# Kernel optimization log

Hardware: AMD Instinct MI355X
Metric: run time of the kernel (lower is better)

Reference implementation:

```python
import jax, jax.numpy as jnp
import numpy as np


def setup_inputs() -> dict:
    B, Lq, Lk, D, F, H = 2, 2048, 2048, 128, 128, 8
    key = jax.random.key(0)
    ks = jax.random.split(key, 8)
    X_Q = jax.random.normal(ks[0], (B, Lq, D), dtype=jnp.float32)
    X_K = jax.random.normal(ks[1], (B, Lk, D), dtype=jnp.float32)
    X_V = jax.random.normal(ks[2], (B, Lk, F), dtype=jnp.float32)
    mask = jax.random.randint(ks[3], (B, 1, Lq, Lk), 0, 2, dtype=jnp.int32)
    # xavier_normal for [H, D, D]: std = sqrt(2/(D+D))
    W_Q = jax.random.normal(ks[4], (H, D, D), dtype=jnp.float32) * np.sqrt(2.0 / (D + D))
    W_K = jax.random.normal(ks[5], (H, D, D), dtype=jnp.float32) * np.sqrt(2.0 / (D + D))
    W_V = jax.random.normal(ks[6], (H, F, F), dtype=jnp.float32) * np.sqrt(2.0 / (F + F))
    O = jax.random.normal(ks[7], (F * H, F), dtype=jnp.float32) * np.sqrt(2.0 / (F * H + F))
    return {"X_Q": X_Q, "X_K": X_K, "X_V": X_V, "mask": mask,
            "W_Q": W_Q, "W_K": W_K, "W_V": W_V, "O": O}


def reference(X_Q, X_K, X_V, mask, W_Q, W_K, W_V, O):
    B, Lq, D = X_Q.shape
    H = W_Q.shape[0]
    F = W_V.shape[1]
    # torch.einsum with repeated in-operand index ('hdd') takes the diagonal
    dq = jnp.diagonal(W_Q, axis1=1, axis2=2)  # [H, D]
    dk = jnp.diagonal(W_K, axis1=1, axis2=2)  # [H, D]
    dv = jnp.diagonal(W_V, axis1=1, axis2=2)  # [H, F]
    g = dq * dk                               # fused per-head QK diagonal scale [H, D]
    scale = 1.0 / jnp.sqrt(jnp.asarray(D, dtype=X_Q.dtype))
    scores = jnp.einsum('bqd,hd,bkd->bhqk', X_Q, g, X_K) * scale  # [B,H,Lq,Lk]
    scores = jnp.where(mask == 0, jnp.asarray(-jnp.inf, scores.dtype), scores)
    A = jax.nn.softmax(scores, axis=-1)
    # O_h = A @ (diag(dv_h) scaled V)
    Oh = jnp.einsum('bhqk,hf,bkf->bhqf', A, dv, X_V)  # [B,H,Lq,F]
    Oh = Oh.transpose(0, 2, 1, 3).reshape(B, Lq, H * F)
    return jnp.einsum('bqx,xf->bqf', Oh, O)
```

## Files before the change

### kernel.cpp

```cpp
#include <hip/hip_runtime.h>

typedef __bf16 bf16;
typedef __bf16 bf16x4 __attribute__((ext_vector_type(4)));
typedef __bf16 bf16x8 __attribute__((ext_vector_type(8)));
typedef float f32x4 __attribute__((ext_vector_type(4)));
typedef short s16x4 __attribute__((ext_vector_type(4)));
typedef unsigned int u32;
typedef unsigned long long u64;

#define B_ 2
#define H_ 8
#define L_ 2048
#define D_ 128
#define F_ 128
#define QT 64
#define KT 64
#define NKT (L_ / KT)

#define WS_KB 0u
#define WS_VT (1u << 20)
#define WS_MB (2u << 20)

#define SMEM_BYTES 66048
#define LWS_OFF 65536
#define POX_STRIDE 132
#define SOH_OFF 36864
#define SOH_STRIDE 136
#define SO2_STRIDE 136

__device__ __forceinline__ void dma16(const void* g, void* l) {
    __builtin_amdgcn_global_load_lds(
        (const __attribute__((address_space(1))) u32*)g,
        (__attribute__((address_space(3))) u32*)l, 16, 0, 0);
}

__device__ __forceinline__ f32x4 mfma32(bf16x8 a, bf16x8 b, f32x4 c) {
    return __builtin_amdgcn_mfma_f32_16x16x32_bf16(a, b, c, 0, 0, 0);
}

__device__ __forceinline__ f32x4 mfma16(bf16x4 a, bf16x4 b, f32x4 c) {
#if __has_builtin(__builtin_amdgcn_mfma_f32_16x16x16_bf16)
    return __builtin_amdgcn_mfma_f32_16x16x16_bf16(a, b, c, 0, 0, 0);
#else
    s16x4 as = __builtin_bit_cast(s16x4, a);
    s16x4 bs = __builtin_bit_cast(s16x4, b);
    return __builtin_amdgcn_mfma_f32_16x16x16bf16_1k(as, bs, c, 0, 0, 0);
#endif
}

__global__ __launch_bounds__(256)
void prep_all(const float* __restrict__ XK, const float* __restrict__ XV,
              const int* __restrict__ mask, bf16* __restrict__ Kb,
              bf16* __restrict__ Vtb, u64* __restrict__ bits)
{
    const int bid = blockIdx.x;
    const int tid = threadIdx.x;
    if (bid < 8192) {
        int wv = bid * 4 + (tid >> 6);
        int lane = tid & 63;
        size_t base = (size_t)wv * 256;
        #pragma unroll
        for (int s = 0; s < 4; ++s) {
            int m = mask[base + s * 64 + lane];
            u64 bal = __ballot(m != 0);
            if (lane == 0) bits[(size_t)wv * 4 + s] = bal;
        }
    } else if (bid < 8448) {
        int gid = (bid - 8192) * 256 + tid;
        int row = gid >> 4;
        int j   = gid & 15;
        const float* src = XK + (size_t)row * 128 + j * 8;
        float4 v0 = *(const float4*)src;
        float4 v1 = *(const float4*)(src + 4);
        bf16x8 w;
        w[0] = (bf16)v0.x; w[1] = (bf16)v0.y; w[2] = (bf16)v0.z; w[3] = (bf16)v0.w;
        w[4] = (bf16)v1.x; w[5] = (bf16)v1.y; w[6] = (bf16)v1.z; w[7] = (bf16)v1.w;
        int jp = j ^ (row & 15);
        *(bf16x8*)(Kb + (size_t)row * 128 + jp * 8) = w;
    } else {
        int idx  = bid - 8448;
        int tile = idx >> 2;
        int fq   = idx & 3;
        int f    = fq * 32 + (tid & 31);
        int j    = tid >> 5;
        int bb   = tile >> 5, kt = tile & 31;
        const float* src = XV + ((size_t)(bb * L_ + kt * 64 + j * 8)) * F_ + f;
        bf16x4 w0, w1;
        #pragma unroll
        for (int jj = 0; jj < 4; ++jj) {
            w0[jj] = (bf16)src[(size_t)jj * F_];
            w1[jj] = (bf16)src[(size_t)(4 + jj) * F_];
        }
        bf16* outp = Vtb + (size_t)tile * 8192 + f * 64;
        *(bf16x4*)(outp + (((2 * j) ^ (f & 15)) * 4)) = w0;
        *(bf16x4*)(outp + (((2 * j + 1) ^ (f & 15)) * 4)) = w1;
    }
}

__global__ __launch_bounds__(512, 4)
void attn_fused_kernel(const float* __restrict__ XQ, const bf16* __restrict__ Kb,
                       const bf16* __restrict__ Vtb, const u64* __restrict__ bits,
                       const float* __restrict__ WQ, const float* __restrict__ WK,
                       const float* __restrict__ WV, const float* __restrict__ Om,
                       float* __restrict__ out)
{
    __shared__ __align__(16) char smem[SMEM_BYTES];
    __shared__ __align__(16) float g_s[128];

    bf16* sK0 = (bf16*)smem;
    bf16* sK1 = (bf16*)(smem + 16384);
    bf16* sV0 = (bf16*)(smem + 32768);
    bf16* sV1 = (bf16*)(smem + 49152);
    float* lws = (float*)(smem + LWS_OFF);
    float* pOx = (float*)smem;
    bf16* sOh  = (bf16*)(smem + SOH_OFF);
    bf16* sO2t = (bf16*)smem;

    const int tid  = threadIdx.x;
    const int wave = tid >> 6;
    const int lane = tid & 63;
    const int c    = lane & 15;
    const int quad = lane >> 4;
    const int qt = blockIdx.x, h = blockIdx.y, b = blockIdx.z;
    const int q0 = qt * QT;

    const int kh   = wave >> 2;
    const int msel = wave & 3;
    const int fv  = tid & 127;
    const int grp = tid >> 7;

    if (tid < 128) {
        float wq = WQ[(h * D_ + tid) * D_ + tid];
        float wk = WK[(h * D_ + tid) * D_ + tid];
        g_s[tid] = wq * wk * 0.08838834764831845f;
    }
    __syncthreads();

    const char* gKbase = (const char*)Kb + (size_t)(b * L_) * 256;
    const char* gVbase = (const char*)Vtb + (size_t)(b * NKT) * 16384;

    #pragma unroll
    for (int i = 0; i < 2; ++i) dma16(gKbase + i * 8192 + tid * 16, (char*)sK0 + i * 8192 + tid * 16);
    #pragma unroll
    for (int i = 0; i < 2; ++i) dma16(gVbase + i * 8192 + tid * 16, (char*)sV0 + i * 8192 + tid * 16);

    bf16x8 qfrag[4];
    {
        const float* qrow = XQ + (size_t)(b * L_ + q0 + msel * 16 + c) * D_;
        #pragma unroll
        for (int kc = 0; kc < 4; ++kc) {
            int d0 = kc * 32 + quad * 8;
            float4 v0 = *(const float4*)(qrow + d0);
            float4 v1 = *(const float4*)(qrow + d0 + 4);
            float4 g0 = *(const float4*)(g_s + d0);
            float4 g1 = *(const float4*)(g_s + d0 + 4);
            bf16x8 w;
            w[0] = (bf16)(v0.x * g0.x); w[1] = (bf16)(v0.y * g0.y);
            w[2] = (bf16)(v0.z * g0.z); w[3] = (bf16)(v0.w * g0.w);
            w[4] = (bf16)(v1.x * g1.x); w[5] = (bf16)(v1.y * g1.y);
            w[6] = (bf16)(v1.z * g1.z); w[7] = (bf16)(v1.w * g1.w);
            qfrag[kc] = w;
        }
    }

    f32x4 oacc[8];
    #pragma unroll
    for (int fi = 0; fi < 8; ++fi)
        #pragma unroll
        for (int r = 0; r < 4; ++r) oacc[fi][r] = 0.f;
    float lsum = 0.f;

    const u64* mrow = bits + (size_t)(b * L_ + q0 + msel * 16 + c) * NKT;

    #pragma unroll 2
    for (int kt = 0; kt < NKT; ++kt) {
        bf16* sK  = (kt & 1) ? sK1 : sK0;
        bf16* sV  = (kt & 1) ? sV1 : sV0;
        bf16* sKn = (kt & 1) ? sK0 : sK1;
        bf16* sVn = (kt & 1) ? sV0 : sV1;

        asm volatile("s_barrier" ::: "memory");

        u64 mb = mrow[kt];

        if (kt + 1 < NKT) {
            const char* gk = gKbase + (size_t)(kt + 1) * 16384;
            const char* gv = gVbase + (size_t)(kt + 1) * 16384;
            #pragma unroll
            for (int i = 0; i < 2; ++i) dma16(gk + i * 8192 + tid * 16, (char*)sKn + i * 8192 + tid * 16);
            #pragma unroll
            for (int i = 0; i < 2; ++i) dma16(gv + i * 8192 + tid * 16, (char*)sVn + i * 8192 + tid * 16);
            asm volatile("s_waitcnt vmcnt(5)" ::: "memory");
        } else {
            asm volatile("s_waitcnt vmcnt(1)" ::: "memory");
        }
        asm volatile("s_barrier" ::: "memory");

        f32x4 tacc[2];
        #pragma unroll
        for (int kti = 0; kti < 2; ++kti)
            #pragma unroll
            for (int r = 0; r < 4; ++r) tacc[kti][r] = 0.f;

        #pragma unroll
        for (int kti = 0; kti < 2; ++kti) {
            const bf16* krow = sK + ((kh * 2 + kti) * 16 + c) * 128;
            #pragma unroll
            for (int kc = 0; kc < 4; ++kc) {
                bf16x8 kfrag = *(const bf16x8*)(krow + (((kc * 4 + quad) ^ c) * 8));
                tacc[kti] = mfma32(kfrag, qfrag[kc], tacc[kti]);
            }
        }

        bf16x4 pfrag[2];
        #pragma unroll
        for (int kti = 0; kti < 2; ++kti) {
            #pragma unroll
            for (int r = 0; r < 4; ++r) {
                float p = ((mb >> (kh * 32 + kti * 16 + quad * 4 + r)) & 1ull)
                          ? __expf(tacc[kti][r]) : 0.f;
                lsum += p;
                pfrag[kti][r] = (bf16)p;
            }
        }

        #pragma unroll
        for (int fi = 0; fi < 8; ++fi) {
            #pragma unroll
            for (int kti = 0; kti < 2; ++kti) {
                int g = kh * 8 + kti * 4 + quad;
                bf16x4 vfrag = *(const bf16x4*)(sV + (fi * 16 + c) * 64 + ((g ^ c) * 4));
                oacc[fi] = mfma16(pfrag[kti], vfrag, oacc[fi]);
            }
        }
    }

    {
        float v = lsum;
        v += __shfl_xor(v, 16); v += __shfl_xor(v, 32);
        if (lane < 16) lws[wave * 16 + lane] = v;
    }
    if (tid < 128)
        g_s[tid] = WV[(h * F_ + tid) * F_ + tid];
    __syncthreads();

    if (kh == 1) {
        #pragma unroll
        for (int fi = 0; fi < 8; ++fi)
            #pragma unroll
            for (int r = 0; r < 4; ++r)
                pOx[(msel * 16 + quad * 4 + r) * POX_STRIDE + fi * 16 + c] = oacc[fi][r];
    }
    __syncthreads();

    if (kh == 0) {
        float linv[4];
        #pragma unroll
        for (int r = 0; r < 4; ++r) {
            int m16 = quad * 4 + r;
            linv[r] = 1.0f / (lws[msel * 16 + m16] + lws[(4 + msel) * 16 + m16]);
        }
        #pragma unroll
        for (int fi = 0; fi < 8; ++fi)
            #pragma unroll
            for (int r = 0; r < 4; ++r) {
                int row = msel * 16 + quad * 4 + r;
                float v = (oacc[fi][r] + pOx[row * POX_STRIDE + fi * 16 + c]) * linv[r];
                sOh[row * SOH_STRIDE + fi * 16 + c] = (bf16)v;
            }
    }
    __syncthreads();

    #pragma unroll
    for (int i = 0; i < 8; ++i) {
        int fp4 = grp * 32 + i * 4;
        bf16x4 w;
        #pragma unroll
        for (int j = 0; j < 4; ++j) {
            int x = fp4 + j;
            w[j] = (bf16)(Om[(h * F_ + x) * F_ + fv] * g_s[x]);
        }
        *(bf16x4*)(sO2t + fv * SO2_STRIDE + fp4) = w;
    }
    __syncthreads();

    const int pm = wave & 3;
    const int pf = wave >> 2;
    bf16x8 afr[4];
    const bf16* ohrow = sOh + (pm * 16 + c) * SOH_STRIDE;
    #pragma unroll
    for (int kc = 0; kc < 4; ++kc)
        afr[kc] = *(const bf16x8*)(ohrow + kc * 32 + quad * 8);

    #pragma unroll
    for (int nt = 0; nt < 4; ++nt) {
        f32x4 pacc;
        #pragma unroll
        for (int r = 0; r < 4; ++r) pacc[r] = 0.f;
        const bf16* orow = sO2t + ((pf * 4 + nt) * 16 + c) * SO2_STRIDE;
        #pragma unroll
        for (int kc = 0; kc < 4; ++kc) {
            bf16x8 bfrag = *(const bf16x8*)(orow + kc * 32 + quad * 8);
            pacc = mfma32(afr[kc], bfrag, pacc);
        }
        #pragma unroll
        for (int r = 0; r < 4; ++r) {
            int qg = q0 + pm * 16 + quad * 4 + r;
            atomicAdd(out + ((size_t)(b * L_ + qg) * F_ + (pf * 4 + nt) * 16 + c), pacc[r]);
        }
    }
}

extern "C" void kernel_launch(void* const* d_in, const int* in_sizes, int n_in,
                              void* d_out, int out_size, void* d_ws, size_t ws_size,
                              hipStream_t stream) {
    const float* XQ   = (const float*)d_in[0];
    const float* XK   = (const float*)d_in[1];
    const float* XV   = (const float*)d_in[2];
    const int*   mask = (const int*)d_in[3];
    const float* WQ   = (const float*)d_in[4];
    const float* WK   = (const float*)d_in[5];
    const float* WV   = (const float*)d_in[6];
    const float* Om   = (const float*)d_in[7];
    float* out = (float*)d_out;

    char* ws = (char*)d_ws;
    bf16* Kb   = (bf16*)(ws + WS_KB);
    bf16* Vtb  = (bf16*)(ws + WS_VT);
    u64*  bits = (u64*)(ws + WS_MB);

    prep_all<<<8704, 256, 0, stream>>>(XK, XV, mask, Kb, Vtb, bits);
    hipMemsetAsync(out, 0, (size_t)out_size * sizeof(float), stream);

    dim3 grid(L_ / QT, H_, B_);
    attn_fused_kernel<<<grid, 512, 0, stream>>>(XQ, Kb, Vtb, bits, WQ, WK, WV, Om, out);
}
```

Baseline: 156.0 us.

## Double query tile per block, load V fragments directly to registers, use exp2

Result: slower. 180.8 us (+15.9%).

```diff
diff --git a/kernel.cpp b/kernel.cpp
--- a/kernel.cpp
+++ b/kernel.cpp
@@ -13,20 +13,22 @@
 #define L_ 2048
 #define D_ 128
 #define F_ 128
-#define QT 64
+#define QT 128
 #define KT 64
 #define NKT (L_ / KT)
+#define NQT (L_ / QT)
 
 #define WS_KB 0u
 #define WS_VT (1u << 20)
 #define WS_MB (2u << 20)
 
-#define SMEM_BYTES 66048
-#define LWS_OFF 65536
+#define SMEM_BYTES 136192
+#define POX_OFF 32768
 #define POX_STRIDE 132
-#define SOH_OFF 36864
+#define SOH_OFF 100352
 #define SOH_STRIDE 136
 #define SO2_STRIDE 136
+#define LWS_OFF 135168
 
 __device__ __forceinline__ void dma16(const void* g, void* l) {
     __builtin_amdgcn_global_load_lds(
@@ -45,6 +47,14 @@
     s16x4 as = __builtin_bit_cast(s16x4, a);
     s16x4 bs = __builtin_bit_cast(s16x4, b);
     return __builtin_amdgcn_mfma_f32_16x16x16bf16_1k(as, bs, c, 0, 0, 0);
+#endif
+}
+
+__device__ __forceinline__ float fast_exp2(float x) {
+#if __has_builtin(__builtin_amdgcn_exp2f)
+    return __builtin_amdgcn_exp2f(x);
+#else
+    return exp2f(x);
 #endif
 }
 
@@ -78,26 +88,29 @@
         int jp = j ^ (row & 15);
         *(bf16x8*)(Kb + (size_t)row * 128 + jp * 8) = w;
     } else {
-        int idx  = bid - 8448;
-        int tile = idx >> 2;
-        int fq   = idx & 3;
-        int f    = fq * 32 + (tid & 31);
-        int j    = tid >> 5;
-        int bb   = tile >> 5, kt = tile & 31;
-        const float* src = XV + ((size_t)(bb * L_ + kt * 64 + j * 8)) * F_ + f;
-        bf16x4 w0, w1;
-        #pragma unroll
-        for (int jj = 0; jj < 4; ++jj) {
-            w0[jj] = (bf16)src[(size_t)jj * F_];
-            w1[jj] = (bf16)src[(size_t)(4 + jj) * F_];
-        }
-        bf16* outp = Vtb + (size_t)tile * 8192 + f * 64;
-        *(bf16x4*)(outp + (((2 * j) ^ (f & 15)) * 4)) = w0;
-        *(bf16x4*)(outp + (((2 * j + 1) ^ (f & 15)) * 4)) = w1;
-    }
-}
-
-__global__ __launch_bounds__(512, 4)
+        int tile = bid - 8448;
+        int bb = tile >> 5, kt = tile & 31;
+        #pragma unroll
+        for (int i = 0; i < 4; ++i) {
+            int idx  = tid * 4 + i;
+            int fblk = idx >> 6;
+            int lane = idx & 63;
+            int c = lane & 15, quad = lane >> 4;
+            int fi = fblk >> 1, kh = fblk & 1;
+            int f = fi * 16 + c;
+            int kb = kt * 64 + kh * 32 + quad * 4;
+            bf16x8 w;
+            #pragma unroll
+            for (int j = 0; j < 4; ++j) {
+                w[j]     = (bf16)XV[(size_t)(bb * L_ + kb + j) * F_ + f];
+                w[4 + j] = (bf16)XV[(size_t)(bb * L_ + kb + 16 + j) * F_ + f];
+            }
+            *(bf16x8*)(Vtb + (size_t)tile * 8192 + fblk * 512 + lane * 8) = w;
+        }
+    }
+}
+
+__global__ __launch_bounds__(512, 2)
 void attn_fused_kernel(const float* __restrict__ XQ, const bf16* __restrict__ Kb,
                        const bf16* __restrict__ Vtb, const u64* __restrict__ bits,
                        const float* __restrict__ WQ, const float* __restrict__ WK,
@@ -107,14 +120,12 @@
     __shared__ __align__(16) char smem[SMEM_BYTES];
     __shared__ __align__(16) float g_s[128];
 
-    bf16* sK0 = (bf16*)smem;
-    bf16* sK1 = (bf16*)(smem + 16384);
-    bf16* sV0 = (bf16*)(smem + 32768);
-    bf16* sV1 = (bf16*)(smem + 49152);
+    bf16* sK0  = (bf16*)smem;
+    bf16* sK1  = (bf16*)(smem + 16384);
+    float* pOx = (float*)(smem + POX_OFF);
+    bf16* sO2t = (bf16*)(smem + POX_OFF);
+    bf16* sOh  = (bf16*)(smem + SOH_OFF);
     float* lws = (float*)(smem + LWS_OFF);
-    float* pOx = (float*)smem;
-    bf16* sOh  = (bf16*)(smem + SOH_OFF);
-    bf16* sO2t = (bf16*)smem;
 
     const int tid  = threadIdx.x;
     const int wave = tid >> 6;
@@ -132,21 +143,20 @@
     if (tid < 128) {
         float wq = WQ[(h * D_ + tid) * D_ + tid];
         float wk = WK[(h * D_ + tid) * D_ + tid];
-        g_s[tid] = wq * wk * 0.08838834764831845f;
-    }
-    __syncthreads();
-
-    const char* gKbase = (const char*)Kb + (size_t)(b * L_) * 256;
-    const char* gVbase = (const char*)Vtb + (size_t)(b * NKT) * 16384;
-
-    #pragma unroll
-    for (int i = 0; i < 2; ++i) dma16(gKbase + i * 8192 + tid * 16, (char*)sK0 + i * 8192 + tid * 16);
-    #pragma unroll
-    for (int i = 0; i < 2; ++i) dma16(gVbase + i * 8192 + tid * 16, (char*)sV0 + i * 8192 + tid * 16);
-
-    bf16x8 qfrag[4];
-    {
-        const float* qrow = XQ + (size_t)(b * L_ + q0 + msel * 16 + c) * D_;
+        g_s[tid] = wq * wk * 0.12752230502179406f;
+    }
+    __syncthreads();
+
+    const char* gK = (const char*)Kb + (size_t)(b * L_) * 256;
+    const char* gV = (const char*)Vtb + (size_t)(b * NKT) * 16384;
+
+    dma16(gK + tid * 16, (char*)sK0 + tid * 16);
+    dma16(gK + 8192 + tid * 16, (char*)sK0 + 8192 + tid * 16);
+
+    bf16x8 qfrag[2][4];
+    #pragma unroll
+    for (int mi = 0; mi < 2; ++mi) {
+        const float* qrow = XQ + (size_t)(b * L_ + q0 + msel * 32 + mi * 16 + c) * D_;
         #pragma unroll
         for (int kc = 0; kc < 4; ++kc) {
             int d0 = kc * 32 + quad * 8;
@@ -159,48 +169,56 @@
             w[2] = (bf16)(v0.z * g0.z); w[3] = (bf16)(v0.w * g0.w);
             w[4] = (bf16)(v1.x * g1.x); w[5] = (bf16)(v1.y * g1.y);
             w[6] = (bf16)(v1.z * g1.z); w[7] = (bf16)(v1.w * g1.w);
-            qfrag[kc] = w;
-        }
-    }
-
-    f32x4 oacc[8];
-    #pragma unroll
-    for (int fi = 0; fi < 8; ++fi)
-        #pragma unroll
-        for (int r = 0; r < 4; ++r) oacc[fi][r] = 0.f;
-    float lsum = 0.f;
-
-    const u64* mrow = bits + (size_t)(b * L_ + q0 + msel * 16 + c) * NKT;
+            qfrag[mi][kc] = w;
+        }
+    }
+
+    f32x4 oacc[2][8];
+    #pragma unroll
+    for (int mi = 0; mi < 2; ++mi)
+        #pragma unroll
+        for (int fi = 0; fi < 8; ++fi)
+            #pragma unroll
+            for (int r = 0; r < 4; ++r) oacc[mi][fi][r] = 0.f;
+    float lsum[2] = {0.f, 0.f};
+
+    const u64* mrow0 = bits + (size_t)(b * L_ + q0 + msel * 32 + c) * NKT;
+    const u64* mrow1 = mrow0 + (size_t)16 * NKT;
 
     #pragma unroll 2
     for (int kt = 0; kt < NKT; ++kt) {
         bf16* sK  = (kt & 1) ? sK1 : sK0;
-        bf16* sV  = (kt & 1) ? sV1 : sV0;
         bf16* sKn = (kt & 1) ? sK0 : sK1;
-        bf16* sVn = (kt & 1) ? sV0 : sV1;
 
         asm volatile("s_barrier" ::: "memory");
 
-        u64 mb = mrow[kt];
+        bf16x8 vload[8];
+        {
+            const char* gvt = gV + (size_t)kt * 16384 + kh * 1024 + lane * 16;
+            #pragma unroll
+            for (int fi = 0; fi < 8; ++fi)
+                vload[fi] = *(const bf16x8*)(gvt + fi * 2048);
+        }
+        u64 mb0 = mrow0[kt];
+        u64 mb1 = mrow1[kt];
 
         if (kt + 1 < NKT) {
-            const char* gk = gKbase + (size_t)(kt + 1) * 16384;
-            const char* gv = gVbase + (size_t)(kt + 1) * 16384;
-            #pragma unroll
-            for (int i = 0; i < 2; ++i) dma16(gk + i * 8192 + tid * 16, (char*)sKn + i * 8192 + tid * 16);
-            #pragma unroll
-            for (int i = 0; i < 2; ++i) dma16(gv + i * 8192 + tid * 16, (char*)sVn + i * 8192 + tid * 16);
-            asm volatile("s_waitcnt vmcnt(5)" ::: "memory");
+            const char* gkn = gK + (size_t)(kt + 1) * 16384;
+            dma16(gkn + tid * 16, (char*)sKn + tid * 16);
+            dma16(gkn + 8192 + tid * 16, (char*)sKn + 8192 + tid * 16);
+            asm volatile("s_waitcnt vmcnt(12)" ::: "memory");
         } else {
-            asm volatile("s_waitcnt vmcnt(1)" ::: "memory");
+            asm volatile("s_waitcnt vmcnt(10)" ::: "memory");
         }
         asm volatile("s_barrier" ::: "memory");
 
-        f32x4 tacc[2];
-        #pragma unroll
-        for (int kti = 0; kti < 2; ++kti)
-            #pragma unroll
-            for (int r = 0; r < 4; ++r) tacc[kti][r] = 0.f;
+        f32x4 tacc[2][2];
+        #pragma unroll
+        for (int mi = 0; mi < 2; ++mi)
+            #pragma unroll
+            for (int kti = 0; kti < 2; ++kti)
+                #pragma unroll
+                for (int r = 0; r < 4; ++r) tacc[mi][kti][r] = 0.f;
 
         #pragma unroll
         for (int kti = 0; kti < 2; ++kti) {
@@ -208,37 +226,44 @@
             #pragma unroll
             for (int kc = 0; kc < 4; ++kc) {
                 bf16x8 kfrag = *(const bf16x8*)(krow + (((kc * 4 + quad) ^ c) * 8));
-                tacc[kti] = mfma32(kfrag, qfrag[kc], tacc[kti]);
-            }
-        }
-
-        bf16x4 pfrag[2];
-        #pragma unroll
-        for (int kti = 0; kti < 2; ++kti) {
-            #pragma unroll
-            for (int r = 0; r < 4; ++r) {
-                float p = ((mb >> (kh * 32 + kti * 16 + quad * 4 + r)) & 1ull)
-                          ? __expf(tacc[kti][r]) : 0.f;
-                lsum += p;
-                pfrag[kti][r] = (bf16)p;
+                tacc[0][kti] = mfma32(kfrag, qfrag[0][kc], tacc[0][kti]);
+                tacc[1][kti] = mfma32(kfrag, qfrag[1][kc], tacc[1][kti]);
+            }
+        }
+
+        bf16x4 pfrag[2][2];
+        #pragma unroll
+        for (int mi = 0; mi < 2; ++mi) {
+            u64 mb = mi ? mb1 : mb0;
+            #pragma unroll
+            for (int kti = 0; kti < 2; ++kti) {
+                #pragma unroll
+                for (int r = 0; r < 4; ++r) {
+                    int pos = kh * 32 + kti * 16 + quad * 4 + r;
+                    float p = ((mb >> pos) & 1ull) ? fast_exp2(tacc[mi][kti][r]) : 0.f;
+                    lsum[mi] += p;
+                    pfrag[mi][kti][r] = (bf16)p;
+                }
             }
         }
 
         #pragma unroll
         for (int fi = 0; fi < 8; ++fi) {
-            #pragma unroll
-            for (int kti = 0; kti < 2; ++kti) {
-                int g = kh * 8 + kti * 4 + quad;
-                bf16x4 vfrag = *(const bf16x4*)(sV + (fi * 16 + c) * 64 + ((g ^ c) * 4));
-                oacc[fi] = mfma16(pfrag[kti], vfrag, oacc[fi]);
-            }
-        }
-    }
-
-    {
-        float v = lsum;
+            bf16x4 v0 = __builtin_shufflevector(vload[fi], vload[fi], 0, 1, 2, 3);
+            bf16x4 v1 = __builtin_shufflevector(vload[fi], vload[fi], 4, 5, 6, 7);
+            #pragma unroll
+            for (int mi = 0; mi < 2; ++mi) {
+                oacc[mi][fi] = mfma16(pfrag[mi][0], v0, oacc[mi][fi]);
+                oacc[mi][fi] = mfma16(pfrag[mi][1], v1, oacc[mi][fi]);
+            }
+        }
+    }
+
+    #pragma unroll
+    for (int mi = 0; mi < 2; ++mi) {
+        float v = lsum[mi];
         v += __shfl_xor(v, 16); v += __shfl_xor(v, 32);
-        if (lane < 16) lws[wave * 16 + lane] = v;
+        if (lane < 16) lws[wave * 32 + mi * 16 + lane] = v;
     }
     if (tid < 128)
         g_s[tid] = WV[(h * F_ + tid) * F_ + tid];
@@ -246,28 +271,34 @@
 
     if (kh == 1) {
         #pragma unroll
-        for (int fi = 0; fi < 8; ++fi)
-            #pragma unroll
-            for (int r = 0; r < 4; ++r)
-                pOx[(msel * 16 + quad * 4 + r) * POX_STRIDE + fi * 16 + c] = oacc[fi][r];
+        for (int mi = 0; mi < 2; ++mi)
+            #pragma unroll
+            for (int fi = 0; fi < 8; ++fi)
+                #pragma unroll
+                for (int r = 0; r < 4; ++r)
+                    pOx[(msel * 32 + mi * 16 + quad * 4 + r) * POX_STRIDE + fi * 16 + c]
+                        = oacc[mi][fi][r];
     }
     __syncthreads();
 
     if (kh == 0) {
-        float linv[4];
-        #pragma unroll
-        for (int r = 0; r < 4; ++r) {
-            int m16 = quad * 4 + r;
-            linv[r] = 1.0f / (lws[msel * 16 + m16] + lws[(4 + msel) * 16 + m16]);
-        }
-        #pragma unroll
-        for (int fi = 0; fi < 8; ++fi)
+        #pragma unroll
+        for (int mi = 0; mi < 2; ++mi) {
+            float linv[4];
             #pragma unroll
             for (int r = 0; r < 4; ++r) {
-                int row = msel * 16 + quad * 4 + r;
-                float v = (oacc[fi][r] + pOx[row * POX_STRIDE + fi * 16 + c]) * linv[r];
-                sOh[row * SOH_STRIDE + fi * 16 + c] = (bf16)v;
-            }
+                int s = mi * 16 + quad * 4 + r;
+                linv[r] = 1.0f / (lws[msel * 32 + s] + lws[(4 + msel) * 32 + s]);
+            }
+            #pragma unroll
+            for (int fi = 0; fi < 8; ++fi)
+                #pragma unroll
+                for (int r = 0; r < 4; ++r) {
+                    int row = msel * 32 + mi * 16 + quad * 4 + r;
+                    float v = (oacc[mi][fi][r] + pOx[row * POX_STRIDE + fi * 16 + c]) * linv[r];
+                    sOh[row * SOH_STRIDE + fi * 16 + c] = (bf16)v;
+                }
+        }
     }
     __syncthreads();
 
@@ -284,8 +315,7 @@
     }
     __syncthreads();
 
-    const int pm = wave & 3;
-    const int pf = wave >> 2;
+    const int pm = wave;
     bf16x8 afr[4];
     const bf16* ohrow = sOh + (pm * 16 + c) * SOH_STRIDE;
     #pragma unroll
@@ -293,11 +323,11 @@
         afr[kc] = *(const bf16x8*)(ohrow + kc * 32 + quad * 8);
 
     #pragma unroll
-    for (int nt = 0; nt < 4; ++nt) {
+    for (int nt = 0; nt < 8; ++nt) {
         f32x4 pacc;
         #pragma unroll
         for (int r = 0; r < 4; ++r) pacc[r] = 0.f;
-        const bf16* orow = sO2t + ((pf * 4 + nt) * 16 + c) * SO2_STRIDE;
+        const bf16* orow = sO2t + (nt * 16 + c) * SO2_STRIDE;
         #pragma unroll
         for (int kc = 0; kc < 4; ++kc) {
             bf16x8 bfrag = *(const bf16x8*)(orow + kc * 32 + quad * 8);
@@ -306,7 +336,7 @@
         #pragma unroll
         for (int r = 0; r < 4; ++r) {
             int qg = q0 + pm * 16 + quad * 4 + r;
-            atomicAdd(out + ((size_t)(b * L_ + qg) * F_ + (pf * 4 + nt) * 16 + c), pacc[r]);
+            atomicAdd(out + ((size_t)(b * L_ + qg) * F_ + nt * 16 + c), pacc[r]);
         }
     }
 }
@@ -329,9 +359,9 @@
     bf16* Vtb  = (bf16*)(ws + WS_VT);
     u64*  bits = (u64*)(ws + WS_MB);
 
-    prep_all<<<8704, 256, 0, stream>>>(XK, XV, mask, Kb, Vtb, bits);
+    prep_all<<<8512, 256, 0, stream>>>(XK, XV, mask, Kb, Vtb, bits);
     hipMemsetAsync(out, 0, (size_t)out_size * sizeof(float), stream);
 
-    dim3 grid(L_ / QT, H_, B_);
+    dim3 grid(NQT, H_, B_);
     attn_fused_kernel<<<grid, 512, 0, stream>>>(XQ, Kb, Vtb, bits, WQ, WK, WV, Om, out);
 }
```

## Prepack K/V in MFMA fragment order and read directly from global, dropping LDS staging

Applied to the files above, without the earlier changes.

Result: slower. 224.2 us (+43.7%).

```diff
diff --git a/kernel.cpp b/kernel.cpp
--- a/kernel.cpp
+++ b/kernel.cpp
@@ -16,23 +16,18 @@
 #define QT 64
 #define KT 64
 #define NKT (L_ / KT)
+#define NQT (L_ / QT)
 
 #define WS_KB 0u
 #define WS_VT (1u << 20)
 #define WS_MB (2u << 20)
 
-#define SMEM_BYTES 66048
-#define LWS_OFF 65536
+#define SMEM_BYTES 52736
 #define POX_STRIDE 132
-#define SOH_OFF 36864
+#define SOH_OFF 34816
 #define SOH_STRIDE 136
 #define SO2_STRIDE 136
-
-__device__ __forceinline__ void dma16(const void* g, void* l) {
-    __builtin_amdgcn_global_load_lds(
-        (const __attribute__((address_space(1))) u32*)g,
-        (__attribute__((address_space(3))) u32*)l, 16, 0, 0);
-}
+#define LWS_OFF 52224
 
 __device__ __forceinline__ f32x4 mfma32(bf16x8 a, bf16x8 b, f32x4 c) {
     return __builtin_amdgcn_mfma_f32_16x16x32_bf16(a, b, c, 0, 0, 0);
@@ -45,6 +40,14 @@
     s16x4 as = __builtin_bit_cast(s16x4, a);
     s16x4 bs = __builtin_bit_cast(s16x4, b);
     return __builtin_amdgcn_mfma_f32_16x16x16bf16_1k(as, bs, c, 0, 0, 0);
+#endif
+}
+
+__device__ __forceinline__ float fast_exp2(float x) {
+#if __has_builtin(__builtin_amdgcn_exp2f)
+    return __builtin_amdgcn_exp2f(x);
+#else
+    return exp2f(x);
 #endif
 }
 
@@ -65,35 +68,45 @@
             u64 bal = __ballot(m != 0);
             if (lane == 0) bits[(size_t)wv * 4 + s] = bal;
         }
-    } else if (bid < 8448) {
-        int gid = (bid - 8192) * 256 + tid;
-        int row = gid >> 4;
-        int j   = gid & 15;
-        const float* src = XK + (size_t)row * 128 + j * 8;
-        float4 v0 = *(const float4*)src;
-        float4 v1 = *(const float4*)(src + 4);
-        bf16x8 w;
-        w[0] = (bf16)v0.x; w[1] = (bf16)v0.y; w[2] = (bf16)v0.z; w[3] = (bf16)v0.w;
-        w[4] = (bf16)v1.x; w[5] = (bf16)v1.y; w[6] = (bf16)v1.z; w[7] = (bf16)v1.w;
-        int jp = j ^ (row & 15);
-        *(bf16x8*)(Kb + (size_t)row * 128 + jp * 8) = w;
+    } else if (bid < 8256) {
+        int tile = bid - 8192;
+        int bb = tile >> 5, kt = tile & 31;
+        #pragma unroll
+        for (int i = 0; i < 4; ++i) {
+            int idx  = tid * 4 + i;
+            int frag = idx >> 6;
+            int lane = idx & 63;
+            int c = lane & 15, quad = lane >> 4;
+            int kti = frag >> 2, kc = frag & 3;
+            const float* src = XK + (size_t)(bb * L_ + kt * 64 + kti * 16 + c) * D_
+                               + kc * 32 + quad * 8;
+            float4 v0 = *(const float4*)src;
+            float4 v1 = *(const float4*)(src + 4);
+            bf16x8 w;
+            w[0] = (bf16)v0.x; w[1] = (bf16)v0.y; w[2] = (bf16)v0.z; w[3] = (bf16)v0.w;
+            w[4] = (bf16)v1.x; w[5] = (bf16)v1.y; w[6] = (bf16)v1.z; w[7] = (bf16)v1.w;
+            *(bf16x8*)(Kb + (size_t)tile * 8192 + frag * 512 + lane * 8) = w;
+        }
     } else {
-        int idx  = bid - 8448;
-        int tile = idx >> 2;
-        int fq   = idx & 3;
-        int f    = fq * 32 + (tid & 31);
-        int j    = tid >> 5;
-        int bb   = tile >> 5, kt = tile & 31;
-        const float* src = XV + ((size_t)(bb * L_ + kt * 64 + j * 8)) * F_ + f;
-        bf16x4 w0, w1;
-        #pragma unroll
-        for (int jj = 0; jj < 4; ++jj) {
-            w0[jj] = (bf16)src[(size_t)jj * F_];
-            w1[jj] = (bf16)src[(size_t)(4 + jj) * F_];
-        }
-        bf16* outp = Vtb + (size_t)tile * 8192 + f * 64;
-        *(bf16x4*)(outp + (((2 * j) ^ (f & 15)) * 4)) = w0;
-        *(bf16x4*)(outp + (((2 * j + 1) ^ (f & 15)) * 4)) = w1;
+        int tile = bid - 8256;
+        int bb = tile >> 5, kt = tile & 31;
+        #pragma unroll
+        for (int i = 0; i < 4; ++i) {
+            int idx  = tid * 4 + i;
+            int frag = idx >> 6;
+            int lane = idx & 63;
+            int c = lane & 15, quad = lane >> 4;
+            int fi = frag >> 1, kp = frag & 1;
+            const float* src = XV + (size_t)(bb * L_ + kt * 64 + kp * 32 + quad * 4) * F_
+                               + fi * 16 + c;
+            bf16x8 w;
+            #pragma unroll
+            for (int j = 0; j < 4; ++j) {
+                w[j]     = (bf16)src[(size_t)j * F_];
+                w[4 + j] = (bf16)src[(size_t)(16 + j) * F_];
+            }
+            *(bf16x8*)(Vtb + (size_t)tile * 8192 + frag * 512 + lane * 8) = w;
+        }
     }
 }
 
@@ -107,14 +120,10 @@
     __shared__ __align__(16) char smem[SMEM_BYTES];
     __shared__ __align__(16) float g_s[128];
 
-    bf16* sK0 = (bf16*)smem;
-    bf16* sK1 = (bf16*)(smem + 16384);
-    bf16* sV0 = (bf16*)(smem + 32768);
-    bf16* sV1 = (bf16*)(smem + 49152);
+    float* pOx = (float*)smem;
+    bf16* sO2t = (bf16*)smem;
+    bf16* sOh  = (bf16*)(smem + SOH_OFF);
     float* lws = (float*)(smem + LWS_OFF);
-    float* pOx = (float*)smem;
-    bf16* sOh  = (bf16*)(smem + SOH_OFF);
-    bf16* sO2t = (bf16*)smem;
 
     const int tid  = threadIdx.x;
     const int wave = tid >> 6;
@@ -124,25 +133,20 @@
     const int qt = blockIdx.x, h = blockIdx.y, b = blockIdx.z;
     const int q0 = qt * QT;
 
-    const int kh   = wave >> 2;
-    const int msel = wave & 3;
+    const int msel   = wave & 3;
+    const int kslice = wave >> 2;
     const int fv  = tid & 127;
     const int grp = tid >> 7;
 
     if (tid < 128) {
         float wq = WQ[(h * D_ + tid) * D_ + tid];
         float wk = WK[(h * D_ + tid) * D_ + tid];
-        g_s[tid] = wq * wk * 0.08838834764831845f;
-    }
-    __syncthreads();
-
-    const char* gKbase = (const char*)Kb + (size_t)(b * L_) * 256;
-    const char* gVbase = (const char*)Vtb + (size_t)(b * NKT) * 16384;
-
-    #pragma unroll
-    for (int i = 0; i < 2; ++i) dma16(gKbase + i * 8192 + tid * 16, (char*)sK0 + i * 8192 + tid * 16);
-    #pragma unroll
-    for (int i = 0; i < 2; ++i) dma16(gVbase + i * 8192 + tid * 16, (char*)sV0 + i * 8192 + tid * 16);
+        g_s[tid] = wq * wk * 0.12752230502179406f;
+    }
+    __syncthreads();
+
+    const char* gK = (const char*)Kb + (size_t)b * 524288;
+    const char* gV = (const char*)Vtb + (size_t)b * 524288;
 
     bf16x8 qfrag[4];
     {
@@ -172,66 +176,53 @@
 
     const u64* mrow = bits + (size_t)(b * L_ + q0 + msel * 16 + c) * NKT;
 
-    #pragma unroll 2
-    for (int kt = 0; kt < NKT; ++kt) {
-        bf16* sK  = (kt & 1) ? sK1 : sK0;
-        bf16* sV  = (kt & 1) ? sV1 : sV0;
-        bf16* sKn = (kt & 1) ? sK0 : sK1;
-        bf16* sVn = (kt & 1) ? sV0 : sV1;
-
-        asm volatile("s_barrier" ::: "memory");
-
+    for (int it = 0; it < 16; ++it) {
+        const int kt = kslice + 2 * it;
+        const bf16* kb = (const bf16*)(gK + (size_t)kt * 16384);
+        const bf16* vb = (const bf16*)(gV + (size_t)kt * 16384);
         u64 mb = mrow[kt];
 
-        if (kt + 1 < NKT) {
-            const char* gk = gKbase + (size_t)(kt + 1) * 16384;
-            const char* gv = gVbase + (size_t)(kt + 1) * 16384;
-            #pragma unroll
-            for (int i = 0; i < 2; ++i) dma16(gk + i * 8192 + tid * 16, (char*)sKn + i * 8192 + tid * 16);
-            #pragma unroll
-            for (int i = 0; i < 2; ++i) dma16(gv + i * 8192 + tid * 16, (char*)sVn + i * 8192 + tid * 16);
-            asm volatile("s_waitcnt vmcnt(5)" ::: "memory");
-        } else {
-            asm volatile("s_waitcnt vmcnt(1)" ::: "memory");
-        }
-        asm volatile("s_barrier" ::: "memory");
-
-        f32x4 tacc[2];
-        #pragma unroll
-        for (int kti = 0; kti < 2; ++kti)
+        f32x4 tacc[4];
+        #pragma unroll
+        for (int kti = 0; kti < 4; ++kti)
             #pragma unroll
             for (int r = 0; r < 4; ++r) tacc[kti][r] = 0.f;
 
         #pragma unroll
-        for (int kti = 0; kti < 2; ++kti) {
-            const bf16* krow = sK + ((kh * 2 + kti) * 16 + c) * 128;
-            #pragma unroll
-            for (int kc = 0; kc < 4; ++kc) {
-                bf16x8 kfrag = *(const bf16x8*)(krow + (((kc * 4 + quad) ^ c) * 8));
-                tacc[kti] = mfma32(kfrag, qfrag[kc], tacc[kti]);
+        for (int kti = 0; kti < 4; ++kti) {
+            bf16x8 kf[4];
+            #pragma unroll
+            for (int kc = 0; kc < 4; ++kc)
+                kf[kc] = *(const bf16x8*)(kb + (kti * 4 + kc) * 512 + lane * 8);
+            #pragma unroll
+            for (int kc = 0; kc < 4; ++kc)
+                tacc[kti] = mfma32(kf[kc], qfrag[kc], tacc[kti]);
+        }
+
+        bf16x4 pf[4];
+        #pragma unroll
+        for (int kti = 0; kti < 4; ++kti) {
+            #pragma unroll
+            for (int r = 0; r < 4; ++r) {
+                int pos = kti * 16 + quad * 4 + r;
+                float p = ((mb >> pos) & 1ull) ? fast_exp2(tacc[kti][r]) : 0.f;
+                lsum += p;
+                pf[kti][r] = (bf16)p;
             }
         }
 
-        bf16x4 pfrag[2];
-        #pragma unroll
-        for (int kti = 0; kti < 2; ++kti) {
-            #pragma unroll
-            for (int r = 0; r < 4; ++r) {
-                float p = ((mb >> (kh * 32 + kti * 16 + quad * 4 + r)) & 1ull)
-                          ? __expf(tacc[kti][r]) : 0.f;
-                lsum += p;
-                pfrag[kti][r] = (bf16)p;
-            }
-        }
-
         #pragma unroll
         for (int fi = 0; fi < 8; ++fi) {
-            #pragma unroll
-            for (int kti = 0; kti < 2; ++kti) {
-                int g = kh * 8 + kti * 4 + quad;
-                bf16x4 vfrag = *(const bf16x4*)(sV + (fi * 16 + c) * 64 + ((g ^ c) * 4));
-                oacc[fi] = mfma16(pfrag[kti], vfrag, oacc[fi]);
-            }
+            bf16x8 vp0 = *(const bf16x8*)(vb + (fi * 2 + 0) * 512 + lane * 8);
+            bf16x8 vp1 = *(const bf16x8*)(vb + (fi * 2 + 1) * 512 + lane * 8);
+            bf16x4 a0 = __builtin_shufflevector(vp0, vp0, 0, 1, 2, 3);
+            bf16x4 a1 = __builtin_shufflevector(vp0, vp0, 4, 5, 6, 7);
+            bf16x4 a2 = __builtin_shufflevector(vp1, vp1, 0, 1, 2, 3);
+            bf16x4 a3 = __builtin_shufflevector(vp1, vp1, 4, 5, 6, 7);
+            oacc[fi] = mfma16(pf[0], a0, oacc[fi]);
+            oacc[fi] = mfma16(pf[1], a1, oacc[fi]);
+            oacc[fi] = mfma16(pf[2], a2, oacc[fi]);
+            oacc[fi] = mfma16(pf[3], a3, oacc[fi]);
         }
     }
 
@@ -244,7 +235,7 @@
         g_s[tid] = WV[(h * F_ + tid) * F_ + tid];
     __syncthreads();
 
-    if (kh == 1) {
+    if (kslice == 1) {
         #pragma unroll
         for (int fi = 0; fi < 8; ++fi)
             #pragma unroll
@@ -253,12 +244,12 @@
     }
     __syncthreads();
 
-    if (kh == 0) {
+    if (kslice == 0) {
         float linv[4];
         #pragma unroll
         for (int r = 0; r < 4; ++r) {
-            int m16 = quad * 4 + r;
-            linv[r] = 1.0f / (lws[msel * 16 + m16] + lws[(4 + msel) * 16 + m16]);
+            int s = quad * 4 + r;
+            linv[r] = 1.0f / (lws[msel * 16 + s] + lws[(4 + msel) * 16 + s]);
         }
         #pragma unroll
         for (int fi = 0; fi < 8; ++fi)
@@ -329,9 +320,9 @@
     bf16* Vtb  = (bf16*)(ws + WS_VT);
     u64*  bits = (u64*)(ws + WS_MB);
 
-    prep_all<<<8704, 256, 0, stream>>>(XK, XV, mask, Kb, Vtb, bits);
+    prep_all<<<8320, 256, 0, stream>>>(XK, XV, mask, Kb, Vtb, bits);
     hipMemsetAsync(out, 0, (size_t)out_size * sizeof(float), stream);
 
-    dim3 grid(L_ / QT, H_, B_);
+    dim3 grid(NQT, H_, B_);
     attn_fused_kernel<<<grid, 512, 0, stream>>>(XQ, Kb, Vtb, bits, WQ, WK, WV, Om, out);
 }
```
